# Kernel optimization log

Measured on AMD Instinct MI355X. Metric: run time of the kernel, lower is better.

Reference implementation:

```python
import jax, jax.numpy as jnp
import numpy as np

P = 51        # n_patches per side
PS = 5        # patch size (255 // 51)
H = 8         # n_heads
EPS = 1e-5    # LayerNorm eps


def positional_embeddings(seq_len, d):
    i = jnp.arange(seq_len, dtype=jnp.float32)[:, None]
    j = jnp.arange(d, dtype=jnp.float32)[None, :]
    # even j -> sin(i / 10000**(j/d)); odd j -> cos(i / 10000**((j-1)/d))
    j_even = j - jnp.mod(j, 2.0)
    angle = i / jnp.power(10000.0, j_even / d)
    return jnp.where(jnp.mod(j, 2.0) == 0, jnp.sin(angle), jnp.cos(angle))


def setup_inputs() -> dict:
    key = jax.random.key(0)
    ks = jax.random.split(key, 12)
    E, IN_D, NC = 128, 75, 3
    return {
        "images": jax.random.normal(ks[0], (64, 3, 255, 255), dtype=jnp.float32),
        "lm_w": jax.random.normal(ks[1], (E, IN_D), dtype=jnp.float32) * 0.1,
        "lm_b": jax.random.normal(ks[2], (E,), dtype=jnp.float32) * 0.1,
        "cls_tok": jax.random.uniform(ks[3], (1, E), dtype=jnp.float32),
        "w_in": jax.random.normal(ks[4], (3 * E, E), dtype=jnp.float32) * 0.05,
        "b_in": jax.random.normal(ks[5], (3 * E,), dtype=jnp.float32) * 0.05,
        "w_out": jax.random.normal(ks[6], (E, E), dtype=jnp.float32) * 0.05,
        "b_out": jax.random.normal(ks[7], (E,), dtype=jnp.float32) * 0.05,
        "ln_g": jnp.ones((E,), dtype=jnp.float32),
        "ln_b": jnp.zeros((E,), dtype=jnp.float32),
        "out_w": jax.random.normal(ks[8], (NC, E), dtype=jnp.float32) * 0.1,
        "out_b": jax.random.normal(ks[9], (NC,), dtype=jnp.float32) * 0.1,
    }


def reference(images, lm_w, lm_b, cls_tok, w_in, b_in, w_out, b_out, ln_g, ln_b, out_w, out_b):
    n, c, h, w = images.shape
    E = lm_w.shape[0]
    hd = E // H
    # --- patchify (vectorized equivalent of the triple Python loop) ---
    # flatten order per patch is (c, ph, pw), patches ordered row-major (i, j)
    patches = images.reshape(n, c, P, PS, P, PS)
    patches = patches.transpose(0, 2, 4, 1, 3, 5).reshape(n, P * P, c * PS * PS)
    # --- linear embed + class token + positional embeddings ---
    tokens = patches @ lm_w.T + lm_b                      # (n, P*P, E)
    cls = jnp.broadcast_to(cls_tok[None], (n, 1, E))
    x = jnp.concatenate([cls, tokens], axis=1)            # (n, S, E), S = P*P+1
    S = P * P + 1
    x = x + positional_embeddings(S, E)[None]
    # --- MultiheadAttention, faithful to torch default batch_first=False:
    # torch interprets axis 0 (=n, the image batch) as the SEQUENCE dim and
    # axis 1 (=S tokens) as the batch dim, so attention mixes across images.
    qkv = x @ w_in.T + b_in                               # (n, S, 3E)
    q, k, v = jnp.split(qkv, 3, axis=-1)
    q = q.reshape(n, S, H, hd) * (1.0 / np.sqrt(hd))
    k = k.reshape(n, S, H, hd)
    v = v.reshape(n, S, H, hd)
    scores = jnp.einsum('lshd,mshd->shlm', q, k)          # (S, H, n, n)
    attn = jax.nn.softmax(scores, axis=-1)
    o = jnp.einsum('shlm,mshd->lshd', attn, v).reshape(n, S, E)
    x = o @ w_out.T + b_out                               # (n, S, E)
    # --- LayerNorm (dropout is identity in eval) ---
    mu = jnp.mean(x, axis=-1, keepdims=True)
    var = jnp.mean(jnp.square(x - mu), axis=-1, keepdims=True)
    x = (x - mu) * jax.lax.rsqrt(var + EPS) * ln_g + ln_b
    # --- mean pool over tokens + classifier head ---
    pooled = jnp.mean(x, axis=1)                          # (n, E)
    return pooled @ out_w.T + out_b                       # (n, n_classes)
```

## Files before the change

kernel.cpp:

```cpp
#include <hip/hip_runtime.h>
#include <math.h>

#define NIMG 64
#define SEQ  2602
#define EMB  128
#define HD   16
#define SPAD 2624
#define KQ   96
#define LSQ  104
#define LSO  136
#define PST  80
#define TOK  8

typedef float f32x4 __attribute__((ext_vector_type(4)));
typedef short short8 __attribute__((ext_vector_type(8)));

__device__ __forceinline__ unsigned short f2bf(float f) {
    union { float f; unsigned int u; } v; v.f = f;
    return (unsigned short)((v.u + 0x8000u) >> 16);
}

__global__ __launch_bounds__(128) void build_A(
    const float* __restrict__ lm_b, const float* __restrict__ cls,
    float* __restrict__ A) {
    const int s = blockIdx.x, e = threadIdx.x;
    const bool odd = e & 1;
    float v;
    if (s == 0) {
        v = cls[e] + (odd ? 1.0f : 0.0f);
    } else if (s < SEQ) {
        float pfac = powf(10000.0f, -(float)(e & ~1) / 128.0f);
        float ang = (float)s * pfac;
        v = lm_b[e] + (odd ? cosf(ang) : sinf(ang));
    } else {
        v = 0.0f;
    }
    A[(size_t)s * 128 + e] = v;
}

__global__ __launch_bounds__(128) void build_W2(
    const float* __restrict__ w_in, const float* __restrict__ lm_w,
    unsigned short* __restrict__ W2) {
    const int j = blockIdx.x, f = threadIdx.x;
    if (f >= KQ) return;
    float acc = 0.0f;
    if (f < 75) {
        for (int e = 0; e < 128; ++e)
            acc += w_in[j * 128 + e] * lm_w[e * 75 + f];
    }
    W2[j * KQ + f] = f2bf(acc);
}

__global__ __launch_bounds__(128) void build_Wout(
    const float* __restrict__ w_out, unsigned short* __restrict__ Wo) {
    const int j = blockIdx.x, e = threadIdx.x;
    Wo[j * 128 + e] = f2bf(w_out[j * 128 + e]);
}

__global__ __launch_bounds__(1024) void zero_pooled(float* __restrict__ p) {
    p[blockIdx.x * 1024 + threadIdx.x] = 0.0f;
}

__global__ __launch_bounds__(1024) void zero_cls(unsigned int* __restrict__ p) {
    p[blockIdx.x * 1024 + threadIdx.x] = 0u;
}

__global__ __launch_bounds__(256) void patchify(
    const float* __restrict__ images, unsigned short* __restrict__ Pb) {
    __shared__ unsigned short rows[15][256];
    const int i = blockIdx.x, l = blockIdx.y;
    const int tid = threadIdx.x;

    if (tid < 255) {
        #pragma unroll
        for (int seg = 0; seg < 15; ++seg) {
            int c = seg / 5, rr = seg % 5;
            float v = images[(((size_t)l * 3 + c) * 255 + (i * 5 + rr)) * 255 + tid];
            rows[seg][tid] = f2bf(v);
        }
    }
    __syncthreads();

    const int j = tid >> 2;
    const int part = tid & 3;
    if (j < 51) {
        const int f0 = part * 24;
        __align__(16) unsigned short buf[24];
        #pragma unroll
        for (int u = 0; u < 24; ++u) {
            int f = f0 + u;
            unsigned short v = 0;
            if (f < 75) {
                int c = f / 25, rem = f % 25, rr = rem / 5, cc = rem % 5;
                v = rows[c * 5 + rr][j * 5 + cc];
            }
            buf[u] = v;
        }
        const int s = i * 51 + j + 1;
        unsigned short* dst = Pb + ((size_t)s * 64 + l) * KQ + f0;
        #pragma unroll
        for (int t = 0; t < 3; ++t)
            *(short8*)(dst + t * 8) = *(const short8*)&buf[t * 8];
    }
}

__global__ __launch_bounds__(256) void gemm_qkv_mfma(
    const unsigned short* __restrict__ P, const unsigned short* __restrict__ W2,
    const float* __restrict__ SB, unsigned short* __restrict__ Qh,
    unsigned short* __restrict__ Kh, unsigned short* __restrict__ Vh) {
    __shared__ __align__(16) unsigned short As[64 * LSQ];
    __shared__ __align__(16) unsigned short Bs[64 * LSQ];
    const int tid = threadIdx.x;
    const int xcd = blockIdx.x & 7;
    const int q_ = blockIdx.x >> 3;
    const int s = xcd + (q_ / 6) * 8;
    const int j = q_ % 6;
    if (s >= SEQ) return;
    const int bm = s * 64;
    const int bn = j * 64;
    const int wv = tid >> 6, lane = tid & 63, quad = lane >> 4, col = lane & 15;

    #pragma unroll
    for (int t = 0; t < 3; ++t) {
        int q = tid + t * 256;
        int row = q & 63, c = q >> 6;
        *(float4*)&As[row * LSQ + c * 8] =
            *(const float4*)(P + (size_t)(bm + row) * KQ + c * 8);
        *(float4*)&Bs[row * LSQ + c * 8] =
            *(const float4*)(W2 + (size_t)(bn + row) * KQ + c * 8);
    }
    __syncthreads();

    f32x4 acc[4] = {};
    const int mrow = wv * 16 + col;
    #pragma unroll
    for (int ks = 0; ks < 3; ++ks) {
        const int k0 = ks * 32 + quad * 8;
        short8 a = *(const short8*)&As[mrow * LSQ + k0];
        #pragma unroll
        for (int nt = 0; nt < 4; ++nt) {
            short8 b = *(const short8*)&Bs[(nt * 16 + col) * LSQ + k0];
            acc[nt] = __builtin_amdgcn_mfma_f32_16x16x32_bf16(a, b, acc[nt], 0, 0, 0);
        }
    }

    const float scale = (j < 2) ? 0.125f : 1.0f;
    unsigned short* dst = (j < 2) ? (Qh + (size_t)s * 8192 + j * 4096)
                        : (j < 4) ? (Kh + (size_t)s * 8192 + (j - 2) * 4096)
                                  : (Vh + (size_t)s * 8192 + (j - 4) * 4096);
    const float* brow = SB + (size_t)s * 384 + bn;

    __syncthreads();
    unsigned short* tile = As;
    #pragma unroll
    for (int nt = 0; nt < 4; ++nt) {
        float bv = brow[nt * 16 + col];
        #pragma unroll
        for (int r = 0; r < 4; ++r) {
            int l = wv * 16 + quad * 4 + r;
            int cc = (l * 2 + (col >> 3)) ^ ((l >> 2) & 3);
            tile[nt * 1024 + cc * 8 + (col & 7)] = f2bf((acc[nt][r] + bv) * scale);
        }
    }
    __syncthreads();
    #pragma unroll
    for (int t = 0; t < 2; ++t) {
        int c = tid + t * 256;
        int nt = c >> 7, cc = c & 127, l = cc >> 1;
        int cs = cc ^ ((l >> 2) & 3);
        *(short8*)(dst + (size_t)c * 8) = *(const short8*)&tile[nt * 1024 + cs * 8];
    }
}

__global__ __launch_bounds__(64) void attention_mfma(
    const unsigned short* __restrict__ Qh, const unsigned short* __restrict__ Kh,
    const unsigned short* __restrict__ Vh, unsigned short* __restrict__ O) {
    __shared__ __align__(16) unsigned short Plds[64 * PST];
    __shared__ __align__(16) unsigned short Vlds[16 * 72];
    __shared__ __align__(16) unsigned short Olds[64 * 16];
    const size_t sh = blockIdx.x;
    const int lane = threadIdx.x, quad = lane >> 4, col = lane & 15;
    const unsigned short* qb = Qh + sh * 1024;
    const unsigned short* kb = Kh + sh * 1024;
    const unsigned short* vb = Vh + sh * 1024;

    short8 v0 = *(const short8*)(vb + lane * 16);
    short8 v1 = *(const short8*)(vb + lane * 16 + 8);
    #pragma unroll
    for (int d = 0; d < 8; ++d) {
        Vlds[d * 72 + lane]       = (unsigned short)v0[d];
        Vlds[(d + 8) * 72 + lane] = (unsigned short)v1[d];
    }

    const int koff = (quad & 1) * 8;
    short8 bfr[4];
    #pragma unroll
    for (int nt = 0; nt < 4; ++nt)
        bfr[nt] = *(const short8*)(kb + (size_t)(nt * 16 + col) * 16 + koff);

    f32x4 sc[4][4] = {};
    #pragma unroll
    for (int mt = 0; mt < 4; ++mt) {
        short8 afr = *(const short8*)(qb + (size_t)(mt * 16 + col) * 16 + koff);
        #pragma unroll
        for (int nt = 0; nt < 4; ++nt)
            sc[mt][nt] = __builtin_amdgcn_mfma_f32_16x16x32_bf16(afr, bfr[nt], sc[mt][nt], 0, 0, 0);
    }

    #pragma unroll
    for (int mt = 0; mt < 4; ++mt) {
        #pragma unroll
        for (int r = 0; r < 4; ++r) {
            const int M = mt * 16 + quad * 4 + r;
            const int swz = (M >> 2) & 7;
            #pragma unroll
            for (int nt = 0; nt < 4; ++nt) {
                int jc = (nt * 2 + (col >> 3)) ^ swz;
                Plds[M * PST + jc * 8 + (col & 7)] = f2bf(__expf(sc[mt][nt][r]));
            }
        }
    }
    __syncthreads();

    short8 vfr[2];
    #pragma unroll
    for (int ks = 0; ks < 2; ++ks)
        vfr[ks] = *(const short8*)&Vlds[col * 72 + ks * 32 + quad * 8];
    short8 ones8;
    #pragma unroll
    for (int i = 0; i < 8; ++i) ones8[i] = (short)0x3F80;

    #pragma unroll
    for (int mt = 0; mt < 4; ++mt) {
        f32x4 o = {}, sm = {};
        const int m = mt * 16 + col;
        const int swz = (m >> 2) & 7;
        #pragma unroll
        for (int ks = 0; ks < 2; ++ks) {
            int kcs = (ks * 4 + quad) ^ swz;
            short8 pa = *(const short8*)&Plds[m * PST + kcs * 8];
            o  = __builtin_amdgcn_mfma_f32_16x16x32_bf16(pa, vfr[ks], o, 0, 0, 0);
            sm = __builtin_amdgcn_mfma_f32_16x16x32_bf16(pa, ones8, sm, 0, 0, 0);
        }
        #pragma unroll
        for (int r = 0; r < 4; ++r) {
            float iv = __builtin_amdgcn_rcpf(sm[r]);
            int l = mt * 16 + quad * 4 + r;
            int cc = (l * 2 + (col >> 3)) ^ ((l >> 2) & 3);
            Olds[cc * 8 + (col & 7)] = f2bf(o[r] * iv);
        }
    }
    __syncthreads();

    unsigned short* od = O + sh * 1024;
    #pragma unroll
    for (int jj = 0; jj < 2; ++jj) {
        int cc = lane * 2 + jj;
        int cs = cc ^ ((lane >> 2) & 3);
        *(short8*)(od + cc * 8) = *(const short8*)&Olds[cs * 8];
    }
}

__global__ __launch_bounds__(256) void gemm_out_ln_pool(
    const unsigned short* __restrict__ O, const unsigned short* __restrict__ Wo,
    const float* __restrict__ b_out, const float* __restrict__ ln_g,
    const float* __restrict__ ln_b, float* __restrict__ pooled) {
    __shared__ __align__(16) unsigned short As[2][64 * LSO];
    __shared__ __align__(16) unsigned short Bs[128 * LSO];
    const int tid = threadIdx.x;
    const int s0 = blockIdx.x * TOK;
    const int wv = tid >> 6, lane = tid & 63, quad = lane >> 4, col = lane & 15;

    #pragma unroll
    for (int t = 0; t < 8; ++t) {
        int q = tid + t * 256;
        int row = q >> 4, c = q & 15;
        *(float4*)&Bs[row * LSO + c * 8] =
            *(const float4*)(Wo + (size_t)row * 128 + c * 8);
    }
    #pragma unroll
    for (int t = 0; t < 4; ++t) {
        int q = tid + t * 256;
        int h = q >> 7, rem = q & 127, l = rem >> 1, jj = rem & 1;
        *(short8*)&As[0][l * LSO + h * 16 + jj * 8] =
            *(const short8*)(O + (size_t)s0 * 8192 + (size_t)q * 8);
    }
    __syncthreads();

    float gch[8], bch[8], boch[8];
    #pragma unroll
    for (int nt = 0; nt < 8; ++nt) {
        int ch = nt * 16 + col;
        gch[nt] = ln_g[ch]; bch[nt] = ln_b[ch]; boch[nt] = b_out[ch];
    }
    const int mrow = wv * 16 + col;
    const int l0 = wv * 16 + quad * 4;
    const int nT = (SEQ - s0 < TOK) ? (SEQ - s0) : TOK;
    float accum[8][4] = {};

    for (int tt = 0; tt < nT; ++tt) {
        if (tt + 1 < nT) {
            const size_t sn = s0 + tt + 1;
            #pragma unroll
            for (int t = 0; t < 4; ++t) {
                int q = tid + t * 256;
                int h = q >> 7, rem = q & 127, l = rem >> 1, jj = rem & 1;
                *(short8*)&As[(tt + 1) & 1][l * LSO + h * 16 + jj * 8] =
                    *(const short8*)(O + sn * 8192 + (size_t)q * 8);
            }
        }
        const unsigned short* Ac = As[tt & 1];
        f32x4 acc[8] = {};
        #pragma unroll
        for (int ks = 0; ks < 4; ++ks) {
            const int k0 = ks * 32 + quad * 8;
            short8 a = *(const short8*)&Ac[mrow * LSO + k0];
            #pragma unroll
            for (int nt = 0; nt < 8; ++nt) {
                short8 b = *(const short8*)&Bs[(nt * 16 + col) * LSO + k0];
                acc[nt] = __builtin_amdgcn_mfma_f32_16x16x32_bf16(a, b, acc[nt], 0, 0, 0);
            }
        }
        #pragma unroll
        for (int r = 0; r < 4; ++r) {
            float yv[8];
            float s1 = 0.0f, s2 = 0.0f;
            #pragma unroll
            for (int nt = 0; nt < 8; ++nt) {
                yv[nt] = acc[nt][r] + boch[nt];
                s1 += yv[nt]; s2 += yv[nt] * yv[nt];
            }
            #pragma unroll
            for (int off = 1; off < 16; off <<= 1) {
                s1 += __shfl_xor(s1, off);
                s2 += __shfl_xor(s2, off);
            }
            float mu = s1 * (1.0f / 128.0f);
            float var = s2 * (1.0f / 128.0f) - mu * mu;
            float rinv = rsqrtf(var + 1e-5f);
            #pragma unroll
            for (int nt = 0; nt < 8; ++nt)
                accum[nt][r] += (yv[nt] - mu) * rinv * gch[nt] + bch[nt];
        }
        __syncthreads();
    }

    #pragma unroll
    for (int nt = 0; nt < 8; ++nt)
        #pragma unroll
        for (int r = 0; r < 4; ++r)
            atomicAdd(&pooled[(l0 + r) * 128 + nt * 16 + col], accum[nt][r]);
}

__global__ __launch_bounds__(256) void gemm64(
    const float* __restrict__ A, int lda, const float* __restrict__ B,
    const float* __restrict__ bias, float* __restrict__ C, int ldc) {
    __shared__ float As[64 * 68];
    __shared__ float Bs[64 * 68];
    const int bm = blockIdx.y * 64;
    const int bn = blockIdx.x * 64;
    const int tid = threadIdx.x;
    const int tx = tid & 15, ty = tid >> 4;

    float acc[4][4] = {};

    for (int kk = 0; kk < 128; kk += 64) {
        __syncthreads();
        #pragma unroll
        for (int t = 0; t < 4; ++t) {
            int q = tid + t * 256;
            int row = q & 63, c4 = (q >> 6) << 2;
            float4 va = *(const float4*)(A + (size_t)(bm + row) * lda + kk + c4);
            As[(c4 + 0) * 68 + row] = va.x;
            As[(c4 + 1) * 68 + row] = va.y;
            As[(c4 + 2) * 68 + row] = va.z;
            As[(c4 + 3) * 68 + row] = va.w;
            float4 vb = *(const float4*)(B + (size_t)(bn + row) * 128 + kk + c4);
            Bs[(c4 + 0) * 68 + row] = vb.x;
            Bs[(c4 + 1) * 68 + row] = vb.y;
            Bs[(c4 + 2) * 68 + row] = vb.z;
            Bs[(c4 + 3) * 68 + row] = vb.w;
        }
        __syncthreads();
        #pragma unroll 4
        for (int k = 0; k < 64; ++k) {
            float4 av = *(const float4*)&As[k * 68 + (ty << 2)];
            float4 bv = *(const float4*)&Bs[k * 68 + (tx << 2)];
            acc[0][0] += av.x*bv.x; acc[0][1] += av.x*bv.y; acc[0][2] += av.x*bv.z; acc[0][3] += av.x*bv.w;
            acc[1][0] += av.y*bv.x; acc[1][1] += av.y*bv.y; acc[1][2] += av.y*bv.z; acc[1][3] += av.y*bv.w;
            acc[2][0] += av.z*bv.x; acc[2][1] += av.z*bv.y; acc[2][2] += av.z*bv.z; acc[2][3] += av.z*bv.w;
            acc[3][0] += av.w*bv.x; acc[3][1] += av.w*bv.y; acc[3][2] += av.w*bv.z; acc[3][3] += av.w*bv.w;
        }
    }

    float4 bv = *(const float4*)(bias + bn + (tx << 2));
    #pragma unroll
    for (int i = 0; i < 4; ++i) {
        float4 r;
        r.x = acc[i][0] + bv.x; r.y = acc[i][1] + bv.y;
        r.z = acc[i][2] + bv.z; r.w = acc[i][3] + bv.w;
        *(float4*)(C + (size_t)(bm + (ty << 2) + i) * ldc + bn + (tx << 2)) = r;
    }
}

__global__ __launch_bounds__(128) void classify(
    const float* __restrict__ pooled, const float* __restrict__ out_w,
    const float* __restrict__ out_b, float* __restrict__ out) {
    const int l = blockIdx.x, e = threadIdx.x;
    __shared__ float sp[EMB];
    sp[e] = pooled[l * EMB + e] * (1.0f / (float)SEQ);
    __syncthreads();
    if (e < 3) {
        float acc = out_b[e];
        #pragma unroll 16
        for (int k = 0; k < EMB; ++k) acc += sp[k] * out_w[e * EMB + k];
        out[l * 3 + e] = acc;
    }
}

extern "C" void kernel_launch(void* const* d_in, const int* in_sizes, int n_in,
                              void* d_out, int out_size, void* d_ws, size_t ws_size,
                              hipStream_t stream) {
    const float* images = (const float*)d_in[0];
    const float* lm_w   = (const float*)d_in[1];
    const float* lm_b   = (const float*)d_in[2];
    const float* cls    = (const float*)d_in[3];
    const float* w_in   = (const float*)d_in[4];
    const float* b_in   = (const float*)d_in[5];
    const float* w_out  = (const float*)d_in[6];
    const float* b_out  = (const float*)d_in[7];
    const float* ln_g   = (const float*)d_in[8];
    const float* ln_b   = (const float*)d_in[9];
    const float* out_w  = (const float*)d_in[10];
    const float* out_b  = (const float*)d_in[11];
    float* out = (float*)d_out;

    float* SB     = (float*)d_ws;
    float* A_pre  = SB + (size_t)SPAD * 384;
    float* pooled = A_pre + (size_t)SPAD * 128;
    unsigned short* W2   = (unsigned short*)(pooled + 64 * 128);
    unsigned short* Wout = W2 + (size_t)384 * KQ;
    unsigned short* Pb   = Wout + 128 * 128;
    unsigned short* Qh   = Pb + (size_t)SEQ * 64 * KQ;
    unsigned short* Kh   = Qh + (size_t)SEQ * 8192;
    unsigned short* Vh   = Kh + (size_t)SEQ * 8192;
    unsigned short* Obuf = Vh + (size_t)SEQ * 8192;

    build_A<<<dim3(SPAD), 128, 0, stream>>>(lm_b, cls, A_pre);
    gemm64<<<dim3(6, SPAD / 64), 256, 0, stream>>>(A_pre, 128, w_in, b_in, SB, 384);
    build_W2<<<dim3(384), 128, 0, stream>>>(w_in, lm_w, W2);
    build_Wout<<<dim3(128), 128, 0, stream>>>(w_out, Wout);
    zero_pooled<<<dim3(8), 1024, 0, stream>>>(pooled);
    zero_cls<<<dim3(3), 1024, 0, stream>>>((unsigned int*)Pb);

    patchify<<<dim3(51, 64), 256, 0, stream>>>(images, Pb);
    gemm_qkv_mfma<<<dim3(8 * 326 * 6), 256, 0, stream>>>(Pb, W2, SB, Qh, Kh, Vh);
    attention_mfma<<<dim3(SEQ * 8), 64, 0, stream>>>(Qh, Kh, Vh, Obuf);
    gemm_out_ln_pool<<<dim3((SEQ + TOK - 1) / TOK), 256, 0, stream>>>(
        Obuf, Wout, b_out, ln_g, ln_b, pooled);
    classify<<<dim3(NIMG), 128, 0, stream>>>(pooled, out_w, out_b, out);
}
```

Baseline: 249.2 us.

## Fuse QKV projection and per-token attention into one kernel

Merges the QKV GEMM and the attention kernel into a single kernel with one block per token, where each wave computes Q/K/V for two heads and keeps them in LDS. This removes the round trip of the Q, K and V intermediates through global memory (about 3×SEQ×8192 bf16) and one kernel launch. In exchange the A and W2 fragments are read straight from global memory without LDS staging, and per-wave LDS use and register pressure (a 6×4 accumulator array) rise, which may lower occupancy. The XCD-aware block remapping is also dropped.

```diff
diff --git a/kernel.cpp b/kernel.cpp
--- a/kernel.cpp
+++ b/kernel.cpp
@@ -7,9 +7,7 @@
 #define HD   16
 #define SPAD 2624
 #define KQ   96
-#define LSQ  104
 #define LSO  136
-#define PST  80
 #define TOK  8
 
 typedef float f32x4 __attribute__((ext_vector_type(4)));
@@ -104,160 +102,132 @@
     }
 }
 
-__global__ __launch_bounds__(256) void gemm_qkv_mfma(
-    const unsigned short* __restrict__ P, const unsigned short* __restrict__ W2,
-    const float* __restrict__ SB, unsigned short* __restrict__ Qh,
-    unsigned short* __restrict__ Kh, unsigned short* __restrict__ Vh) {
-    __shared__ __align__(16) unsigned short As[64 * LSQ];
-    __shared__ __align__(16) unsigned short Bs[64 * LSQ];
+__global__ __launch_bounds__(256) void qkv_attn(
+    const unsigned short* __restrict__ Pb, const unsigned short* __restrict__ W2,
+    const float* __restrict__ SB, unsigned short* __restrict__ Obuf) {
+    __shared__ __align__(16) unsigned short Qw_[4][64 * 40];
+    __shared__ __align__(16) unsigned short Kw_[4][64 * 40];
+    __shared__ __align__(16) unsigned short Vw_[4][32 * 72];
+    __shared__ __align__(16) unsigned short Pw_[4][64 * 80];
+    __shared__ __align__(16) unsigned short Ow_[4][64 * 16];
+
+    const int s = blockIdx.x;
     const int tid = threadIdx.x;
-    const int xcd = blockIdx.x & 7;
-    const int q_ = blockIdx.x >> 3;
-    const int s = xcd + (q_ / 6) * 8;
-    const int j = q_ % 6;
-    if (s >= SEQ) return;
-    const int bm = s * 64;
-    const int bn = j * 64;
-    const int wv = tid >> 6, lane = tid & 63, quad = lane >> 4, col = lane & 15;
-
-    #pragma unroll
-    for (int t = 0; t < 3; ++t) {
-        int q = tid + t * 256;
-        int row = q & 63, c = q >> 6;
-        *(float4*)&As[row * LSQ + c * 8] =
-            *(const float4*)(P + (size_t)(bm + row) * KQ + c * 8);
-        *(float4*)&Bs[row * LSQ + c * 8] =
-            *(const float4*)(W2 + (size_t)(bn + row) * KQ + c * 8);
-    }
-    __syncthreads();
-
-    f32x4 acc[4] = {};
-    const int mrow = wv * 16 + col;
+    const int w = tid >> 6, lane = tid & 63, quad = lane >> 4, col = lane & 15;
+    unsigned short* Qw = Qw_[w];
+    unsigned short* Kw = Kw_[w];
+    unsigned short* Vw = Vw_[w];
+    unsigned short* Pw = Pw_[w];
+    unsigned short* Ow = Ow_[w];
+
+    f32x4 acc[6][4] = {};
+    const unsigned short* arow0 = Pb + (size_t)s * 64 * KQ;
     #pragma unroll
     for (int ks = 0; ks < 3; ++ks) {
         const int k0 = ks * 32 + quad * 8;
-        short8 a = *(const short8*)&As[mrow * LSQ + k0];
-        #pragma unroll
-        for (int nt = 0; nt < 4; ++nt) {
-            short8 b = *(const short8*)&Bs[(nt * 16 + col) * LSQ + k0];
-            acc[nt] = __builtin_amdgcn_mfma_f32_16x16x32_bf16(a, b, acc[nt], 0, 0, 0);
-        }
-    }
-
-    const float scale = (j < 2) ? 0.125f : 1.0f;
-    unsigned short* dst = (j < 2) ? (Qh + (size_t)s * 8192 + j * 4096)
-                        : (j < 4) ? (Kh + (size_t)s * 8192 + (j - 2) * 4096)
-                                  : (Vh + (size_t)s * 8192 + (j - 4) * 4096);
-    const float* brow = SB + (size_t)s * 384 + bn;
-
-    __syncthreads();
-    unsigned short* tile = As;
-    #pragma unroll
-    for (int nt = 0; nt < 4; ++nt) {
-        float bv = brow[nt * 16 + col];
-        #pragma unroll
-        for (int r = 0; r < 4; ++r) {
-            int l = wv * 16 + quad * 4 + r;
-            int cc = (l * 2 + (col >> 3)) ^ ((l >> 2) & 3);
-            tile[nt * 1024 + cc * 8 + (col & 7)] = f2bf((acc[nt][r] + bv) * scale);
-        }
-    }
-    __syncthreads();
-    #pragma unroll
-    for (int t = 0; t < 2; ++t) {
-        int c = tid + t * 256;
-        int nt = c >> 7, cc = c & 127, l = cc >> 1;
-        int cs = cc ^ ((l >> 2) & 3);
-        *(short8*)(dst + (size_t)c * 8) = *(const short8*)&tile[nt * 1024 + cs * 8];
-    }
-}
-
-__global__ __launch_bounds__(64) void attention_mfma(
-    const unsigned short* __restrict__ Qh, const unsigned short* __restrict__ Kh,
-    const unsigned short* __restrict__ Vh, unsigned short* __restrict__ O) {
-    __shared__ __align__(16) unsigned short Plds[64 * PST];
-    __shared__ __align__(16) unsigned short Vlds[16 * 72];
-    __shared__ __align__(16) unsigned short Olds[64 * 16];
-    const size_t sh = blockIdx.x;
-    const int lane = threadIdx.x, quad = lane >> 4, col = lane & 15;
-    const unsigned short* qb = Qh + sh * 1024;
-    const unsigned short* kb = Kh + sh * 1024;
-    const unsigned short* vb = Vh + sh * 1024;
-
-    short8 v0 = *(const short8*)(vb + lane * 16);
-    short8 v1 = *(const short8*)(vb + lane * 16 + 8);
-    #pragma unroll
-    for (int d = 0; d < 8; ++d) {
-        Vlds[d * 72 + lane]       = (unsigned short)v0[d];
-        Vlds[(d + 8) * 72 + lane] = (unsigned short)v1[d];
+        short8 b[6];
+        #pragma unroll
+        for (int nt = 0; nt < 6; ++nt) {
+            int ch = (nt >> 1) * 128 + 32 * w + (nt & 1) * 16 + col;
+            b[nt] = *(const short8*)(W2 + (size_t)ch * KQ + k0);
+        }
+        #pragma unroll
+        for (int mt = 0; mt < 4; ++mt) {
+            short8 a = *(const short8*)(arow0 + (size_t)(mt * 16 + col) * KQ + k0);
+            #pragma unroll
+            for (int nt = 0; nt < 6; ++nt)
+                acc[nt][mt] = __builtin_amdgcn_mfma_f32_16x16x32_bf16(a, b[nt], acc[nt][mt], 0, 0, 0);
+        }
+    }
+
+    const float* sbrow = SB + (size_t)s * 384;
+    #pragma unroll
+    for (int nt = 0; nt < 6; ++nt) {
+        int ch = (nt >> 1) * 128 + 32 * w + (nt & 1) * 16 + col;
+        float bv = sbrow[ch];
+        int chl = (nt & 1) * 16 + col;
+        #pragma unroll
+        for (int mt = 0; mt < 4; ++mt) {
+            #pragma unroll
+            for (int r = 0; r < 4; ++r) {
+                int m = mt * 16 + quad * 4 + r;
+                float v = acc[nt][mt][r] + bv;
+                if (nt < 2)      Qw[m * 40 + chl] = f2bf(v * 0.125f);
+                else if (nt < 4) Kw[m * 40 + chl] = f2bf(v);
+                else             Vw[chl * 72 + m] = f2bf(v);
+            }
+        }
     }
 
     const int koff = (quad & 1) * 8;
-    short8 bfr[4];
-    #pragma unroll
-    for (int nt = 0; nt < 4; ++nt)
-        bfr[nt] = *(const short8*)(kb + (size_t)(nt * 16 + col) * 16 + koff);
-
-    f32x4 sc[4][4] = {};
-    #pragma unroll
-    for (int mt = 0; mt < 4; ++mt) {
-        short8 afr = *(const short8*)(qb + (size_t)(mt * 16 + col) * 16 + koff);
+    short8 ones8;
+    #pragma unroll
+    for (int i = 0; i < 8; ++i) ones8[i] = (short)0x3F80;
+
+    #pragma unroll
+    for (int hl = 0; hl < 2; ++hl) {
+        const int hoff = hl * 16;
+        short8 bfr[4];
         #pragma unroll
         for (int nt = 0; nt < 4; ++nt)
-            sc[mt][nt] = __builtin_amdgcn_mfma_f32_16x16x32_bf16(afr, bfr[nt], sc[mt][nt], 0, 0, 0);
-    }
-
-    #pragma unroll
-    for (int mt = 0; mt < 4; ++mt) {
-        #pragma unroll
-        for (int r = 0; r < 4; ++r) {
-            const int M = mt * 16 + quad * 4 + r;
-            const int swz = (M >> 2) & 7;
-            #pragma unroll
-            for (int nt = 0; nt < 4; ++nt) {
-                int jc = (nt * 2 + (col >> 3)) ^ swz;
-                Plds[M * PST + jc * 8 + (col & 7)] = f2bf(__expf(sc[mt][nt][r]));
-            }
-        }
-    }
-    __syncthreads();
-
-    short8 vfr[2];
-    #pragma unroll
-    for (int ks = 0; ks < 2; ++ks)
-        vfr[ks] = *(const short8*)&Vlds[col * 72 + ks * 32 + quad * 8];
-    short8 ones8;
-    #pragma unroll
-    for (int i = 0; i < 8; ++i) ones8[i] = (short)0x3F80;
-
-    #pragma unroll
-    for (int mt = 0; mt < 4; ++mt) {
-        f32x4 o = {}, sm = {};
-        const int m = mt * 16 + col;
-        const int swz = (m >> 2) & 7;
-        #pragma unroll
-        for (int ks = 0; ks < 2; ++ks) {
-            int kcs = (ks * 4 + quad) ^ swz;
-            short8 pa = *(const short8*)&Plds[m * PST + kcs * 8];
-            o  = __builtin_amdgcn_mfma_f32_16x16x32_bf16(pa, vfr[ks], o, 0, 0, 0);
-            sm = __builtin_amdgcn_mfma_f32_16x16x32_bf16(pa, ones8, sm, 0, 0, 0);
-        }
-        #pragma unroll
-        for (int r = 0; r < 4; ++r) {
-            float iv = __builtin_amdgcn_rcpf(sm[r]);
-            int l = mt * 16 + quad * 4 + r;
-            int cc = (l * 2 + (col >> 3)) ^ ((l >> 2) & 3);
-            Olds[cc * 8 + (col & 7)] = f2bf(o[r] * iv);
-        }
-    }
-    __syncthreads();
-
-    unsigned short* od = O + sh * 1024;
-    #pragma unroll
-    for (int jj = 0; jj < 2; ++jj) {
-        int cc = lane * 2 + jj;
-        int cs = cc ^ ((lane >> 2) & 3);
-        *(short8*)(od + cc * 8) = *(const short8*)&Olds[cs * 8];
+            bfr[nt] = *(const short8*)&Kw[(nt * 16 + col) * 40 + hoff + koff];
+
+        f32x4 sc[4][4] = {};
+        #pragma unroll
+        for (int mt = 0; mt < 4; ++mt) {
+            short8 afr = *(const short8*)&Qw[(mt * 16 + col) * 40 + hoff + koff];
+            #pragma unroll
+            for (int nt = 0; nt < 4; ++nt)
+                sc[mt][nt] = __builtin_amdgcn_mfma_f32_16x16x32_bf16(afr, bfr[nt], sc[mt][nt], 0, 0, 0);
+        }
+
+        #pragma unroll
+        for (int mt = 0; mt < 4; ++mt) {
+            #pragma unroll
+            for (int r = 0; r < 4; ++r) {
+                const int M = mt * 16 + quad * 4 + r;
+                const int swz = (M >> 2) & 7;
+                #pragma unroll
+                for (int nt = 0; nt < 4; ++nt) {
+                    int jc = (nt * 2 + (col >> 3)) ^ swz;
+                    Pw[M * 80 + jc * 8 + (col & 7)] = f2bf(__expf(sc[mt][nt][r]));
+                }
+            }
+        }
+
+        short8 vfr[2];
+        #pragma unroll
+        for (int ks = 0; ks < 2; ++ks)
+            vfr[ks] = *(const short8*)&Vw[(hoff + col) * 72 + ks * 32 + quad * 8];
+
+        #pragma unroll
+        for (int mt = 0; mt < 4; ++mt) {
+            f32x4 o = {}, sm = {};
+            const int m = mt * 16 + col;
+            const int swz = (m >> 2) & 7;
+            #pragma unroll
+            for (int ks = 0; ks < 2; ++ks) {
+                int kcs = (ks * 4 + quad) ^ swz;
+                short8 pa = *(const short8*)&Pw[m * 80 + kcs * 8];
+                o  = __builtin_amdgcn_mfma_f32_16x16x32_bf16(pa, vfr[ks], o, 0, 0, 0);
+                sm = __builtin_amdgcn_mfma_f32_16x16x32_bf16(pa, ones8, sm, 0, 0, 0);
+            }
+            #pragma unroll
+            for (int r = 0; r < 4; ++r) {
+                float iv = __builtin_amdgcn_rcpf(sm[r]);
+                int l = mt * 16 + quad * 4 + r;
+                int cc = (l * 2 + (col >> 3)) ^ ((l >> 2) & 3);
+                Ow[cc * 8 + (col & 7)] = f2bf(o[r] * iv);
+            }
+        }
+
+        unsigned short* od = Obuf + ((size_t)s * 8 + 2 * w + hl) * 1024;
+        #pragma unroll
+        for (int jj = 0; jj < 2; ++jj) {
+            int cc = lane * 2 + jj;
+            int cs = cc ^ ((lane >> 2) & 3);
+            *(short8*)(od + cc * 8) = *(const short8*)&Ow[cs * 8];
+        }
     }
 }
 
@@ -441,10 +411,7 @@
     unsigned short* W2   = (unsigned short*)(pooled + 64 * 128);
     unsigned short* Wout = W2 + (size_t)384 * KQ;
     unsigned short* Pb   = Wout + 128 * 128;
-    unsigned short* Qh   = Pb + (size_t)SEQ * 64 * KQ;
-    unsigned short* Kh   = Qh + (size_t)SEQ * 8192;
-    unsigned short* Vh   = Kh + (size_t)SEQ * 8192;
-    unsigned short* Obuf = Vh + (size_t)SEQ * 8192;
+    unsigned short* Obuf = Pb + (size_t)SEQ * 64 * KQ;
 
     build_A<<<dim3(SPAD), 128, 0, stream>>>(lm_b, cls, A_pre);
     gemm64<<<dim3(6, SPAD / 64), 256, 0, stream>>>(A_pre, 128, w_in, b_in, SB, 384);
@@ -454,8 +421,7 @@
     zero_cls<<<dim3(3), 1024, 0, stream>>>((unsigned int*)Pb);
 
     patchify<<<dim3(51, 64), 256, 0, stream>>>(images, Pb);
-    gemm_qkv_mfma<<<dim3(8 * 326 * 6), 256, 0, stream>>>(Pb, W2, SB, Qh, Kh, Vh);
-    attention_mfma<<<dim3(SEQ * 8), 64, 0, stream>>>(Qh, Kh, Vh, Obuf);
+    qkv_attn<<<dim3(SEQ), 256, 0, stream>>>(Pb, W2, SB, Obuf);
     gemm_out_ln_pool<<<dim3((SEQ + TOK - 1) / TOK), 256, 0, stream>>>(
         Obuf, Wout, b_out, ln_g, ln_b, pooled);
     classify<<<dim3(NIMG), 128, 0, stream>>>(pooled, out_w, out_b, out);
```

Result: no change. 247.8 us (-0.5%).
